# Kernel optimization log

Hardware: AMD Instinct MI355X
Metric: run time of the kernel (lower is better)

The kernel has to match this reference:

```python
import jax, jax.numpy as jnp
from jax import lax
import numpy as np

B, S, IN = 8, 4096, 64
D, H, K = 512, 8, 3
TCN_CH = [256, 256, 512]
HD = D // H


def setup_inputs() -> dict:
    key = jax.random.key(0)
    ks = iter(jax.random.split(key, 64))
    def nrm(shape, s=0.02):
        return jax.random.normal(next(ks), shape, jnp.float32) * s
    inp = {"x": jax.random.normal(next(ks), (B, S, IN), jnp.float32)}
    inp["W_in"] = nrm((IN, D)); inp["b_in"] = jnp.zeros((D,), jnp.float32)
    chans = [D] + TCN_CH
    for i in range(3):
        cin, cout = chans[i], chans[i + 1]
        inp[f"c1w{i}"] = nrm((cout, cin, K), 0.01); inp[f"c1b{i}"] = jnp.zeros((cout,), jnp.float32)
        inp[f"c2w{i}"] = nrm((cout, cout, K), 0.01); inp[f"c2b{i}"] = jnp.zeros((cout,), jnp.float32)
        if cin != cout:  # downsample 1x1 conv (blocks 0 and 2)
            inp[f"dsw{i}"] = nrm((cout, cin, 1), 0.01); inp[f"dsb{i}"] = jnp.zeros((cout,), jnp.float32)
    inp["W_tcn"] = nrm((TCN_CH[-1], D)); inp["b_tcn"] = jnp.zeros((D,), jnp.float32)
    NL = 2  # attention layers, stacked on leading axis
    for n in ["Wq", "Wk", "Wv", "Wo"]:
        inp[n] = nrm((NL, D, D))
    for n in ["bq", "bk", "bv", "bo", "ln_b"]:
        inp[n] = jnp.zeros((NL, D), jnp.float32)
    inp["ln_g"] = jnp.ones((NL, D), jnp.float32)
    inp["W_out"] = nrm((D, 1)); inp["b_out"] = jnp.zeros((1,), jnp.float32)
    return inp


def _conv(x, w, b, dil, pad):
    # x: (B,C,L), w: (O,I,K)
    y = lax.conv_general_dilated(x, w, (1,), [(pad, pad)], rhs_dilation=(dil,),
                                 dimension_numbers=("NCH", "OIH", "NCH"))
    return y + b[None, :, None]


def _block(t, c1w, c1b, c2w, c2b, ds, dil):
    # TemporalConvBlock: symmetric padding (k-1)*dil on both convs, truncate to input length
    pad = (K - 1) * dil
    o = jax.nn.relu(_conv(t, c1w, c1b, dil, pad))   # length L + pad
    o = _conv(o, c2w, c2b, dil, pad)                # length L + 2*pad
    r = t if ds is None else _conv(t, ds[0], ds[1], 1, 0)
    return jax.nn.relu(o[:, :, : t.shape[2]] + r)


def _layernorm(x, g, b, eps=1e-5):
    mu = x.mean(-1, keepdims=True)
    var = ((x - mu) ** 2).mean(-1, keepdims=True)
    return (x - mu) * lax.rsqrt(var + eps) * g + b


def _forward(x, W_in, b_in, c1w0, c1b0, c2w0, c2b0, dsw0, dsb0,
             c1w1, c1b1, c2w1, c2b1, c1w2, c1b2, c2w2, c2b2, dsw2, dsb2,
             W_tcn, b_tcn, Wq, bq, Wk, bk, Wv, bv, Wo, bo, ln_g, ln_b, W_out, b_out):
    h = x @ W_in + b_in                              # (B,S,D)
    t = jnp.swapaxes(h, 1, 2)                        # (B,D,S)
    t = _block(t, c1w0, c1b0, c2w0, c2b0, (dsw0, dsb0), 1)
    t = _block(t, c1w1, c1b1, c2w1, c2b1, None, 2)
    t = _block(t, c1w2, c1b2, c2w2, c2b2, (dsw2, dsb2), 4)
    h = h + jnp.swapaxes(t, 1, 2) @ W_tcn + b_tcn
    # sinusoidal positional encoding
    pos = jnp.arange(S, dtype=jnp.float32)[:, None]
    div = jnp.exp(jnp.arange(0, D, 2, dtype=jnp.float32) * (-np.log(10000.0) / D))
    pe = jnp.stack([jnp.sin(pos * div), jnp.cos(pos * div)], axis=-1).reshape(S, D)
    h = h + pe[None]
    for l in range(Wq.shape[0]):
        res = h
        def heads(y):  # (B,S,D) -> (B,H,S,HD)
            return y.reshape(B, S, H, HD).transpose(0, 2, 1, 3)
        q = heads(h @ Wq[l] + bq[l])
        k = heads(h @ Wk[l] + bk[l])
        v = heads(h @ Wv[l] + bv[l])
        qf = jax.nn.elu(q) + 1.0
        kf = jax.nn.elu(k) + 1.0
        kv = jnp.einsum("bhnd,bhnm->bhdm", kf, v)            # (B,H,HD,HD)
        out = jnp.einsum("bhnd,bhdm->bhnm", qf, kv)          # (B,H,S,HD)
        norm = jnp.maximum(jnp.einsum("bhnd,bhd->bhn", qf, kf.sum(2)), 1e-6)
        out = out / norm[..., None]
        out = out.transpose(0, 2, 1, 3).reshape(B, S, D)
        h = _layernorm(res + out @ Wo[l] + bo[l], ln_g[l], ln_b[l])
    pooled = h.mean(1)                                       # (B,D)
    return (pooled @ W_out + b_out)[:, 0]                    # (B,)


def reference(x, W_in, b_in, c1w0, c1b0, c2w0, c2b0, dsw0, dsb0,
              c1w1, c1b1, c2w1, c2b1, c1w2, c1b2, c2w2, c2b2, dsw2, dsb2,
              W_tcn, b_tcn, Wq, bq, Wk, bk, Wv, bv, Wo, bo, ln_g, ln_b, W_out, b_out):
    return _forward(x, W_in, b_in, c1w0, c1b0, c2w0, c2b0, dsw0, dsb0,
                    c1w1, c1b1, c2w1, c2b1, c1w2, c1b2, c2w2, c2b2, dsw2, dsb2,
                    W_tcn, b_tcn, Wq, bq, Wk, bk, Wv, bv, Wo, bo, ln_g, ln_b, W_out, b_out)
```

## Files before the change

### kernel.cpp

```cpp
#include <hip/hip_runtime.h>

typedef unsigned short u16;
typedef unsigned int u32;
typedef short bhalf8 __attribute__((ext_vector_type(8)));
typedef float f32x4 __attribute__((ext_vector_type(4)));

#define S_LEN 4096
#define NSEG 30

__device__ __forceinline__ float b2f(u16 h){ return __uint_as_float(((u32)h) << 16); }
__device__ __forceinline__ u16 f2b(float f){
  u32 u = __float_as_uint(f);
  return (u16)((u + 0x7FFFu + ((u >> 16) & 1u)) >> 16);
}
__device__ __forceinline__ u32 cvtpk(float a, float b){
  u32 r; asm("v_cvt_pk_bf16_f32 %0, %1, %2" : "=v"(r) : "v"(a), "v"(b)); return r;
}
__device__ __forceinline__ void unp8(uint4 v, float* f){
  f[0]=__uint_as_float(v.x<<16); f[1]=__uint_as_float(v.x&0xffff0000u);
  f[2]=__uint_as_float(v.y<<16); f[3]=__uint_as_float(v.y&0xffff0000u);
  f[4]=__uint_as_float(v.z<<16); f[5]=__uint_as_float(v.z&0xffff0000u);
  f[6]=__uint_as_float(v.w<<16); f[7]=__uint_as_float(v.w&0xffff0000u);
}
__device__ __forceinline__ void unp4(uint2 v, float* f){
  f[0]=__uint_as_float(v.x<<16); f[1]=__uint_as_float(v.x&0xffff0000u);
  f[2]=__uint_as_float(v.y<<16); f[3]=__uint_as_float(v.y&0xffff0000u);
}

__device__ __forceinline__ size_t taddr(int r, int c, int C){
  return (size_t)(r >> 7) * ((size_t)C << 7) + (size_t)((c >> 5) << 12)
       + ((r & 127) << 5) + (c & 31);
}

__device__ __forceinline__ void gload16(const void* g, void* l){
  __builtin_amdgcn_global_load_lds(
      (__attribute__((address_space(1))) void*)(g),
      (__attribute__((address_space(3))) void*)(l), 16, 0, 0);
}

struct PrepArgs {
  const float* src[NSEG];
  int N[NSEG]; int K[NSEG]; int sn[NSEG]; int sk[NSEG]; unsigned off[NSEG];
};

__global__ __launch_bounds__(256) void prep_w(PrepArgs pa, u16* __restrict__ wb){
  int seg = blockIdx.y;
  int N = pa.N[seg], K = pa.K[seg];
  int ntk = (K + 31) >> 5;
  int tiles = ((N + 31) >> 5) * ntk;
  int tile = blockIdx.x;
  if (tile >= tiles) return;
  int n0 = (tile / ntk) << 5, k0 = (tile % ntk) << 5;
  const float* src = pa.src[seg];
  long sn = pa.sn[seg], sk = pa.sk[seg];
  u16* dst = wb + pa.off[seg];
  int lk = threadIdx.x & 31, ln = threadIdx.x >> 5;
  #pragma unroll
  for (int i = 0; i < 4; ++i){
    int n = n0 + ln + i*8, k = k0 + lk;
    if (n < N && k < K)
      dst[(size_t)n*K + k] = f2b(src[(long)n*sn + (long)k*sk]);
  }
}

__global__ __launch_bounds__(256) void pe_k(float* __restrict__ pe){
  int id = blockIdx.x*256 + threadIdx.x;
  int s = id >> 8, i = id & 255;
  float div = expf((float)i * (-2.0f * 9.210340371976184f / 512.0f));
  float a = (float)s * div;
  pe[(size_t)s*512 + 2*i]   = sinf(a);
  pe[(size_t)s*512 + 2*i+1] = cosf(a);
}

__global__ __launch_bounds__(256) void cvt_k(const float* __restrict__ x, u16* __restrict__ xb, int n){
  int id = blockIdx.x*256 + threadIdx.x;
  if (id < n){
    int r = id >> 6, c = id & 63;
    xb[taddr(r, c, 64)] = f2b(x[id]);
  }
}

template<int NTAPS, int KS1, int KS2>
__global__ __launch_bounds__(256) void gemm_k(
    const u16* __restrict__ A, const u16* __restrict__ W,
    const u16* __restrict__ A2, const u16* __restrict__ W2,
    const float* __restrict__ bias, const float* __restrict__ bias2,
    const float* __restrict__ bias3,
    u16* __restrict__ out, const u16* __restrict__ resb,
    const float* __restrict__ peb, const float* __restrict__ den,
    int N, int CA, int CA2, int dil, int nN, int wbstride, int flags)
{
  constexpr bool MT   = (NTAPS == 3);
  constexpr int HALO  = MT ? 8 : 0;
  constexpr int AR    = MT ? 144 : 128;
  constexpr int DA    = (!MT) ? 4 : ((KS2 > 0) ? 4 : 2);
  constexpr int K     = KS1 << 5;
  constexpr int K2    = KS2 << 5;
  constexpr int TOTAL = MT ? (3*KS1 + KS2) : (KS1 + KS2);
  __shared__ u16 As[DA][AR*32];
  __shared__ u16 Bs[4][128*32];
  const int tid = threadIdx.x;
  const int wave = tid >> 6, lane = tid & 63;
  const int wm = wave >> 1, wn = wave & 1;

  const int nwg = gridDim.x;
  const int lin = blockIdx.x;
  const int swz = (lin & 7) * (nwg >> 3) + (lin >> 3);
  const int mb = swz / nN, nb = swz - mb * nN;
  const int m0 = mb << 7, n0 = nb << 7;
  const bool bnd = (m0 & (S_LEN - 1)) == 0;

  const u16* Ae = (flags & 16) ? (A + (((size_t)(n0 & 511) >> 5) << 12)) : A;

  const int lr4 = lane >> 2, lc4 = lane & 3;
  const int c0 = lane >> 4, fro = lane & 15;

  const f32x4 zf = {0.f, 0.f, 0.f, 0.f};
  const bhalf8 zb = {0,0,0,0,0,0,0,0};
  f32x4 acc[4][4];
  #pragma unroll
  for (int i=0;i<4;++i)
    #pragma unroll
    for (int j=0;j<4;++j) acc[i][j] = zf;

  const u16* Wb = W + (size_t)(m0 >> 12) * (size_t)wbstride;
  const size_t abase  = (size_t)mb * ((size_t)CA  << 7);
  const size_t abase2 = (size_t)mb * ((size_t)CA2 << 7);

  auto STAGE_A = [&](int kb, int ab){
    const size_t tb = abase + ((size_t)kb << 12);
    #pragma unroll
    for (int half = 0; half < 2; ++half){
      int mrow = (wave << 5) + (half << 4) + lr4;
      int i = mrow + HALO;
      int cg = lc4 ^ ((i >> 1) & 3);
      gload16(Ae + tb + mrow*32 + (cg << 3), &As[ab][(HALO + (wave << 5) + (half << 4)) * 32]);
    }
    if (MT && wave == 0 && lane < 32){
      int j = lr4;
      int cg = lc4 ^ ((j >> 1) & 3);
      size_t hb_ = (mb ? abase - ((size_t)CA << 7) : abase) + ((size_t)kb << 12) + (120 + j)*32;
      gload16(Ae + hb_ + (cg << 3), &As[ab][0]);
    }
  };
  auto STAGE_A2 = [&](int t2, int ab){
    const size_t tb = abase2 + ((size_t)t2 << 12);
    #pragma unroll
    for (int half = 0; half < 2; ++half){
      int mrow = (wave << 5) + (half << 4) + lr4;
      int i = mrow + HALO;
      int cg = lc4 ^ ((i >> 1) & 3);
      gload16(A2 + tb + mrow*32 + (cg << 3), &As[ab][(HALO + (wave << 5) + (half << 4)) * 32]);
    }
  };
  auto STAGE_B = [&](const u16* Wt, size_t kstride, int kb, int bb){
    #pragma unroll
    for (int half = 0; half < 2; ++half){
      int i = (wave << 5) + (half << 4) + lr4;
      int cg = lc4 ^ ((i >> 1) & 3);
      gload16(Wt + (size_t)(n0 + i) * kstride + (kb << 5) + (cg << 3),
              &Bs[bb][((wave << 5) + (half << 4)) * 32]);
    }
  };
  auto DO16 = [&](int ab, int bb, int sh, bool mask){
    bhalf8 af[4], bf[4];
    #pragma unroll
    for (int mt = 0; mt < 4; ++mt){
      int r8 = (wm << 6) + (mt << 4) + fro + HALO + sh;
      af[mt] = *(const bhalf8*)&As[ab][r8 * 32 + ((c0 ^ ((r8 >> 1) & 3)) << 3)];
    }
    if (MT && mask && bnd && wm == 0 && fro + sh < 0) af[0] = zb;
    #pragma unroll
    for (int nt = 0; nt < 4; ++nt){
      int rB = (wn << 6) + (nt << 4) + fro;
      bf[nt] = *(const bhalf8*)&Bs[bb][rB * 32 + ((c0 ^ ((rB >> 1) & 3)) << 3)];
    }
    #pragma unroll
    for (int mt = 0; mt < 4; ++mt)
      #pragma unroll
      for (int nt = 0; nt < 4; ++nt)
        acc[mt][nt] = __builtin_amdgcn_mfma_f32_16x16x32_bf16(bf[nt], af[mt], acc[mt][nt], 0, 0, 0);
  };

  if constexpr (!MT){
    auto STG = [&](int s){
      int b = s & 3;
      if (s < KS1){ STAGE_A(s, b); STAGE_B(Wb, (size_t)K, s, b); }
      else if (KS2 > 0){ STAGE_A2(s - KS1, b); STAGE_B(W2, (size_t)K2, s - KS1, b); }
    };
    STG(0);
    if constexpr (TOTAL > 1) STG(1);
    if constexpr (TOTAL > 2) STG(2);
    #pragma unroll
    for (int s = 0; s < TOTAL; ++s){
      if (s + 1 >= TOTAL)      asm volatile("s_waitcnt vmcnt(0)" ::: "memory");
      else if (s + 2 >= TOTAL) asm volatile("s_waitcnt vmcnt(4)" ::: "memory");
      else                     asm volatile("s_waitcnt vmcnt(8)" ::: "memory");
      __builtin_amdgcn_sched_barrier(0);
      __builtin_amdgcn_s_barrier();
      __builtin_amdgcn_sched_barrier(0);
      if (s + 3 < TOTAL) STG(s + 3);
      DO16(s & 3, s & 3, 0, false);
    }
  } else {
    auto STG = [&](int s){
      if (s < 3*KS1){
        int kb = s / 3, tap = s % 3;
        if (tap == 0) STAGE_A(kb, kb & (DA-1));
        STAGE_B(Wb + (size_t)tap * N * K, (size_t)K, kb, s & 3);
      } else if (KS2 > 0){
        int t2 = s - 3*KS1;
        STAGE_A2(t2, (KS1 + t2) & (DA-1));
        STAGE_B(W2, (size_t)K2, t2, s & 3);
      }
    };
    STG(0);
    if constexpr (TOTAL > 1) STG(1);
    if constexpr (TOTAL > 2) STG(2);
    #pragma unroll
    for (int s = 0; s < TOTAL; ++s){
      if (s + 1 >= TOTAL)      asm volatile("s_waitcnt vmcnt(0)" ::: "memory");
      else if (s + 2 >= TOTAL) asm volatile("s_waitcnt vmcnt(2)" ::: "memory");
      else                     asm volatile("s_waitcnt vmcnt(4)" ::: "memory");
      __builtin_amdgcn_sched_barrier(0);
      __builtin_amdgcn_s_barrier();
      __builtin_amdgcn_sched_barrier(0);
      if (s + 3 < TOTAL) STG(s + 3);
      if (s < 3*KS1) DO16((s/3) & (DA-1), s & 3, ((s%3) - 2) * dil, true);
      else           DO16((KS1 + (s - 3*KS1)) & (DA-1), s & 3, 0, false);
    }
  }

  const int mb_l = (wm << 6) + fro;
  const int cb_l = (wn << 6) + (c0 << 2);
  const int th = n0 >> 9;
  #pragma unroll
  for (int mt = 0; mt < 4; ++mt){
    const int row = m0 + mb_l + (mt << 4);
    const size_t prow = (size_t)(row & (S_LEN - 1)) * 512;
    #pragma unroll
    for (int nt = 0; nt < 4; ++nt){
      const int col = n0 + cb_l + (nt << 4);
      float v0 = acc[mt][nt][0], v1 = acc[mt][nt][1], v2 = acc[mt][nt][2], v3 = acc[mt][nt][3];
      if (flags & 32){
        const float* bp = (th == 0) ? bias : ((th == 1) ? bias2 : bias3);
        if (bp){ float4 b4 = *(const float4*)&bp[col & 511]; v0+=b4.x; v1+=b4.y; v2+=b4.z; v3+=b4.w; }
      } else {
        if (bias) { float4 b4 = *(const float4*)&bias[col];  v0+=b4.x; v1+=b4.y; v2+=b4.z; v3+=b4.w; }
        if (bias2){ float4 b4 = *(const float4*)&bias2[col]; v0+=b4.x; v1+=b4.y; v2+=b4.z; v3+=b4.w; }
      }
      if (flags & 4){
        uint2 rv = *(const uint2*)(resb + taddr(row, col, N));
        float rf[4]; unp4(rv, rf);
        v0 += rf[0]; v1 += rf[1]; v2 += rf[2]; v3 += rf[3];
      }
      if (flags & 8){
        float4 p4 = *(const float4*)&peb[prow + col];
        v0 += p4.x; v1 += p4.y; v2 += p4.z; v3 += p4.w;
      }
      if (flags & 16){
        float d = fmaxf(den[((size_t)row << 3) + (col >> 6)], 1e-6f);
        float rd = 1.0f / d;
        v0 *= rd; v1 *= rd; v2 *= rd; v3 *= rd;
      }
      if (flags & 1){
        v0 = fmaxf(v0, 0.f); v1 = fmaxf(v1, 0.f); v2 = fmaxf(v2, 0.f); v3 = fmaxf(v3, 0.f);
      }
      if ((flags & 2) && (!(flags & 32) || th < 2)){
        v0 = (v0 > 0.f) ? (v0 + 1.f) : __expf(v0);
        v1 = (v1 > 0.f) ? (v1 + 1.f) : __expf(v1);
        v2 = (v2 > 0.f) ? (v2 + 1.f) : __expf(v2);
        v3 = (v3 > 0.f) ? (v3 + 1.f) : __expf(v3);
      }
      uint2 pk; pk.x = cvtpk(v0, v1); pk.y = cvtpk(v2, v3);
      *(uint2*)(out + taddr(row, col, N)) = pk;
    }
  }
}

__global__ __launch_bounds__(256) void kv_partial(
    const u16* __restrict__ qkv,
    float* __restrict__ kvp, float* __restrict__ ksp)
{
  const int bh = blockIdx.x;
  const int b = bh >> 3, h = bh & 7;
  const int ch = blockIdx.y;
  const int t = threadIdx.x;
  __shared__ u16 kfs[16][64];
  __shared__ u16 vs[16][64];
  float acc[4][4] = {{0.f}};
  float ks[4] = {0.f,0.f,0.f,0.f};
  const int d0 = (t >> 4) << 2;
  const int c0 = (t & 15) << 2;
  const int lr = t >> 4, lc = (t & 15) << 2;
  const int rowbase = (b << 12) + (ch << 9);
  const int ck = 512 + (h << 6) + lc;
  const int cv = 1024 + (h << 6) + lc;
  for (int g = 0; g < 32; ++g){
    int r = rowbase + (g << 4) + lr;
    *(uint2*)&kfs[lr][lc] = *(const uint2*)(qkv + taddr(r, ck, 1536));
    *(uint2*)&vs[lr][lc]  = *(const uint2*)(qkv + taddr(r, cv, 1536));
    __syncthreads();
    #pragma unroll
    for (int i = 0; i < 16; ++i){
      float kv4[4], vv4[4];
      unp4(*(const uint2*)&kfs[i][d0], kv4);
      unp4(*(const uint2*)&vs[i][c0], vv4);
      #pragma unroll
      for (int j=0;j<4;++j)
        #pragma unroll
        for (int k2=0;k2<4;++k2) acc[j][k2] += kv4[j]*vv4[k2];
      if ((t & 15) == 0){
        #pragma unroll
        for (int j=0;j<4;++j) ks[j] += kv4[j];
      }
    }
    __syncthreads();
  }
  float* dst = kvp + ((size_t)(bh << 3) + ch) * 4096;
  #pragma unroll
  for (int j=0;j<4;++j)
    #pragma unroll
    for (int k2=0;k2<4;++k2) dst[(d0+j)*64 + (c0+k2)] = acc[j][k2];
  if ((t & 15) == 0){
    float* kd = ksp + ((size_t)(bh << 3) + ch) * 64;
    #pragma unroll
    for (int j=0;j<4;++j) kd[d0+j] = ks[j];
  }
}

__global__ __launch_bounds__(256) void kvred_k(
    const float* __restrict__ kvp, const float* __restrict__ ksp,
    float* __restrict__ kvf, float* __restrict__ ksf)
{
  int bh = blockIdx.x, t = threadIdx.x;
  for (int e = t; e < 4096; e += 256){
    float s = 0.f;
    #pragma unroll
    for (int ch = 0; ch < 8; ++ch) s += kvp[((size_t)(bh<<3)+ch)*4096 + e];
    kvf[(size_t)bh*4096 + e] = s;
  }
  if (t < 64){
    float s = 0.f;
    #pragma unroll
    for (int ch = 0; ch < 8; ++ch) s += ksp[((size_t)(bh<<3)+ch)*64 + t];
    ksf[bh*64 + t] = s;
  }
}

__global__ __launch_bounds__(256) void den_k(const u16* __restrict__ qkv,
    const float* __restrict__ ksf, float* __restrict__ den)
{
  int id = blockIdx.x*256 + threadIdx.x;
  int r = id >> 3, h = id & 7;
  int b = r >> 12;
  const float* ks = ksf + ((b<<3)+h)*64;
  float s = 0.f;
  for (int d = 0; d < 64; d += 8){
    uint4 vq = *(const uint4*)(qkv + taddr(r, (h << 6) + d, 1536));
    float f[8]; unp8(vq, f);
    #pragma unroll
    for (int j=0;j<8;++j) s += f[j]*ks[d+j];
  }
  den[id] = s;
}

__global__ __launch_bounds__(256) void packkv2_k(const float* __restrict__ kvf, u16* __restrict__ wbd){
  int id = blockIdx.x*256 + threadIdx.x;
  int b = id >> 16;
  int n = (id >> 7) & 511, j = id & 127;
  float v = 0.f;
  if ((j >> 6) == ((n >> 6) & 1))
    v = kvf[((size_t)((b<<3)+(n>>6)))*4096 + (j & 63)*64 + (n & 63)];
  wbd[id] = f2b(v);
}

__global__ __launch_bounds__(256) void ln_k(const u16* __restrict__ in,
    const float* __restrict__ g, const float* __restrict__ beta, u16* __restrict__ out)
{
  int wave = threadIdx.x >> 6, lane = threadIdx.x & 63;
  int row = blockIdx.x*4 + wave;
  size_t ad = taddr(row, lane*8, 512);
  uint4 pv = *(const uint4*)(in + ad);
  float f[8]; unp8(pv, f);
  float s = 0.f, ss = 0.f;
  #pragma unroll
  for (int i=0;i<8;++i){ s += f[i]; ss += f[i]*f[i]; }
  for (int m=1;m<64;m<<=1){ s += __shfl_xor(s,m); ss += __shfl_xor(ss,m); }
  float mean = s * (1.f/512.f);
  float var = ss * (1.f/512.f) - mean*mean;
  float rstd = rsqrtf(fmaxf(var, 0.f) + 1e-5f);
  u16 o[8];
  #pragma unroll
  for (int i=0;i<8;++i){
    int c = lane*8 + i;
    o[i] = f2b((f[i]-mean)*rstd*g[c] + beta[c]);
  }
  *(uint4*)(out + ad) = *(uint4*)o;
}

__global__ __launch_bounds__(256) void pool1_k(const u16* __restrict__ hb,
    const float* __restrict__ wout, float* __restrict__ part)
{
  int b = blockIdx.x >> 6, ch = blockIdx.x & 63;
  int t = threadIdx.x;
  __shared__ float ws[512];
  for (int i=t;i<512;i+=256) ws[i] = wout[i];
  __syncthreads();
  int r = (b << 12) + (ch << 6) + (t >> 2);
  int c0 = (t & 3) << 7;
  float s = 0.f;
  for (int i=0;i<128;i+=8){
    uint4 v = *(const uint4*)(hb + taddr(r, c0 + i, 512));
    float f[8]; unp8(v, f);
    #pragma unroll
    for (int j=0;j<8;++j) s += f[j]*ws[c0+i+j];
  }
  __shared__ float red[256];
  red[t] = s; __syncthreads();
  for (int k=128;k;k>>=1){ if (t<k) red[t]+=red[t+k]; __syncthreads(); }
  if (!t) part[blockIdx.x] = red[0];
}

__global__ __launch_bounds__(64) void pool2_k(const float* __restrict__ part,
    const float* __restrict__ bout, float* __restrict__ out)
{
  int b = blockIdx.x, t = threadIdx.x;
  float s = part[(b << 6) + t];
  for (int m=1;m<64;m<<=1) s += __shfl_xor(s,m);
  if (!t) out[b] = s * (1.f/4096.f) + bout[0];
}

extern "C" void kernel_launch(void* const* d_in, const int* in_sizes, int n_in,
                              void* d_out, int out_size, void* d_ws, size_t ws_size,
                              hipStream_t stream)
{
  (void)in_sizes; (void)n_in; (void)out_size; (void)ws_size;
  const float* x    = (const float*)d_in[0];
  const float* W_in = (const float*)d_in[1];
  const float* b_in = (const float*)d_in[2];
  const float* c1w0 = (const float*)d_in[3];
  const float* c1b0 = (const float*)d_in[4];
  const float* c2w0 = (const float*)d_in[5];
  const float* c2b0 = (const float*)d_in[6];
  const float* dsw0 = (const float*)d_in[7];
  const float* dsb0 = (const float*)d_in[8];
  const float* c1w1 = (const float*)d_in[9];
  const float* c1b1 = (const float*)d_in[10];
  const float* c2w1 = (const float*)d_in[11];
  const float* c2b1 = (const float*)d_in[12];
  const float* c1w2 = (const float*)d_in[13];
  const float* c1b2 = (const float*)d_in[14];
  const float* c2w2 = (const float*)d_in[15];
  const float* c2b2 = (const float*)d_in[16];
  const float* dsw2 = (const float*)d_in[17];
  const float* dsb2 = (const float*)d_in[18];
  const float* W_tcn= (const float*)d_in[19];
  const float* b_tcn= (const float*)d_in[20];
  const float* Wq   = (const float*)d_in[21];
  const float* Wk   = (const float*)d_in[22];
  const float* Wv   = (const float*)d_in[23];
  const float* Wo   = (const float*)d_in[24];
  const float* bq   = (const float*)d_in[25];
  const float* bk   = (const float*)d_in[26];
  const float* bv   = (const float*)d_in[27];
  const float* bo   = (const float*)d_in[28];
  const float* lnb  = (const float*)d_in[29];
  const float* lng  = (const float*)d_in[30];
  const float* W_out= (const float*)d_in[31];
  const float* b_out= (const float*)d_in[32];

  char* base = (char*)d_ws;
  size_t off = 0;
  auto alloc = [&](size_t bytes) -> void* {
    void* p = base + off;
    off += (bytes + 255) & ~(size_t)255;
    return p;
  };
  u16* WB   = (u16*)alloc(4816896ull*2);
  u16* wbd  = (u16*)alloc(8ull*512*128*2);
  float* peb= (float*)alloc(4096ull*512*4);
  float* den= (float*)alloc(32768ull*8*4);
  float* kvp= (float*)alloc(512ull*4096*4);
  float* ksp= (float*)alloc(512ull*64*4);
  float* kvf= (float*)alloc(64ull*4096*4);
  float* ksf= (float*)alloc(64ull*64*4);
  float* part=(float*)alloc(512*4);
  u16* hb   = (u16*)alloc(32768ull*512*2);
  char* qkvR= (char*)alloc(32768ull*1536*2);
  u16* atto = (u16*)alloc(32768ull*512*2);

  u16* qkvb = (u16*)qkvR;
  u16* xb   = (u16*)(qkvR);
  u16* t1b  = (u16*)(qkvR + 4194304);
  u16* t2b  = (u16*)(qkvR + 20971520);
  u16* t3b  = (u16*)(qkvR + 37748736);
  u16* o1b  = atto;

  unsigned wo_ = 0;
  auto wseg = [&](unsigned e){ unsigned o = wo_; wo_ += e; return o; };
  unsigned oWin  = wseg(512*64);
  unsigned oC1w0 = wseg(3*256*512);
  unsigned oC2w0 = wseg(3*256*256);
  unsigned oDs0  = wseg(256*512);
  unsigned oC1w1 = wseg(3*256*256);
  unsigned oC2w1 = wseg(3*256*256);
  unsigned oC1w2 = wseg(3*512*256);
  unsigned oC2w2 = wseg(3*512*512);
  unsigned oDs2  = wseg(512*256);
  unsigned oWtcn = wseg(512*512);
  unsigned oQKV  = wseg(2*1536*512);
  unsigned oWo   = wseg(2*512*512);

  PrepArgs pa;
  int si = 0;
  auto seg = [&](const float* s, int N, int K, int sn, int sk, unsigned o){
    pa.src[si]=s; pa.N[si]=N; pa.K[si]=K; pa.sn[si]=sn; pa.sk[si]=sk; pa.off[si]=o; ++si;
  };
  seg(W_in, 512, 64, 1, 512, oWin);
  for (int t=0;t<3;++t) seg(c1w0 + t, 256, 512, 1536, 3, oC1w0 + t*131072);
  for (int t=0;t<3;++t) seg(c2w0 + t, 256, 256,  768, 3, oC2w0 + t*65536);
  seg(dsw0, 256, 512, 512, 1, oDs0);
  for (int t=0;t<3;++t) seg(c1w1 + t, 256, 256,  768, 3, oC1w1 + t*65536);
  for (int t=0;t<3;++t) seg(c2w1 + t, 256, 256,  768, 3, oC2w1 + t*65536);
  for (int t=0;t<3;++t) seg(c1w2 + t, 512, 256,  768, 3, oC1w2 + t*131072);
  for (int t=0;t<3;++t) seg(c2w2 + t, 512, 512, 1536, 3, oC2w2 + t*262144);
  seg(dsw2, 512, 256, 256, 1, oDs2);
  seg(W_tcn, 512, 512, 1, 512, oWtcn);
  for (int l=0;l<2;++l){
    seg(Wq + l*262144, 512, 512, 1, 512, oQKV + l*786432 + 0);
    seg(Wk + l*262144, 512, 512, 1, 512, oQKV + l*786432 + 262144);
    seg(Wv + l*262144, 512, 512, 1, 512, oQKV + l*786432 + 524288);
  }
  for (int l=0;l<2;++l) seg(Wo + l*262144, 512, 512, 1, 512, oWo + l*262144);

  prep_w<<<dim3(256, NSEG), 256, 0, stream>>>(pa, WB);
  pe_k<<<4096, 256, 0, stream>>>(peb);
  cvt_k<<<8192, 256, 0, stream>>>(x, xb, 32768*64);

  const int RELU=1, ELU1=2, RES=4, PE=8, DIV=16, QKV=32;
  auto gemm = [&](const u16* A, const u16* W, const u16* A2, const u16* W2,
                  const float* b1, const float* b2, const float* b3,
                  u16* out, const u16* resb,
                  int K, int K2, int N, int CA, int CA2, int ntaps,
                  int dil, int wbs, int flags){
    int nN = N >> 7;
    dim3 grid(256 * nN);
    if (ntaps == 3){
      if (K == 512 && K2 == 0)
        gemm_k<3,16,0><<<grid, 256, 0, stream>>>(A, W, A2, W2, b1, b2, b3, out, resb,
                                                 peb, den, N, CA, CA2, dil, nN, wbs, flags);
      else if (K == 256 && K2 == 512)
        gemm_k<3,8,16><<<grid, 256, 0, stream>>>(A, W, A2, W2, b1, b2, b3, out, resb,
                                                 peb, den, N, CA, CA2, dil, nN, wbs, flags);
      else if (K == 256 && K2 == 0)
        gemm_k<3,8,0><<<grid, 256, 0, stream>>>(A, W, A2, W2, b1, b2, b3, out, resb,
                                                peb, den, N, CA, CA2, dil, nN, wbs, flags);
      else
        gemm_k<3,16,8><<<grid, 256, 0, stream>>>(A, W, A2, W2, b1, b2, b3, out, resb,
                                                 peb, den, N, CA, CA2, dil, nN, wbs, flags);
    } else {
      if (K == 64)
        gemm_k<1,2,0><<<grid, 256, 0, stream>>>(A, W, A2, W2, b1, b2, b3, out, resb,
                                                peb, den, N, CA, CA2, dil, nN, wbs, flags);
      else if (K == 128)
        gemm_k<1,4,0><<<grid, 256, 0, stream>>>(A, W, A2, W2, b1, b2, b3, out, resb,
                                                peb, den, N, CA, CA2, dil, nN, wbs, flags);
      else
        gemm_k<1,16,0><<<grid, 256, 0, stream>>>(A, W, A2, W2, b1, b2, b3, out, resb,
                                                 peb, den, N, CA, CA2, dil, nN, wbs, flags);
    }
  };

  gemm(xb, WB + oWin, nullptr, nullptr, b_in, nullptr, nullptr, hb, nullptr,
       64, 0, 512, 64, 0, 1, 1, 0, 0);
  gemm(hb,  WB + oC1w0, nullptr, nullptr, c1b0, nullptr, nullptr, o1b, nullptr,
       512, 0, 256, 512, 0, 3, 1, 0, RELU);
  gemm(o1b, WB + oC2w0, hb, WB + oDs0, c2b0, dsb0, nullptr, t1b, nullptr,
       256, 512, 256, 256, 512, 3, 1, 0, RELU);
  gemm(t1b, WB + oC1w1, nullptr, nullptr, c1b1, nullptr, nullptr, o1b, nullptr,
       256, 0, 256, 256, 0, 3, 2, 0, RELU);
  gemm(o1b, WB + oC2w1, nullptr, nullptr, c2b1, nullptr, nullptr, t2b, t1b,
       256, 0, 256, 256, 0, 3, 2, 0, RELU|RES);
  gemm(t2b, WB + oC1w2, nullptr, nullptr, c1b2, nullptr, nullptr, o1b, nullptr,
       256, 0, 512, 256, 0, 3, 4, 0, RELU);
  gemm(o1b, WB + oC2w2, t2b, WB + oDs2, c2b2, dsb2, nullptr, t3b, nullptr,
       512, 256, 512, 512, 256, 3, 4, 0, RELU);
  gemm(t3b, WB + oWtcn, nullptr, nullptr, b_tcn, nullptr, nullptr, hb, hb,
       512, 0, 512, 512, 0, 1, 1, 0, RES|PE);

  for (int l = 0; l < 2; ++l){
    gemm(hb, WB + oQKV + l*786432, nullptr, nullptr, bq + l*512, bk + l*512, bv + l*512,
         qkvb, nullptr, 512, 0, 1536, 512, 0, 1, 1, 0, ELU1|QKV);
    kv_partial<<<dim3(64, 8), 256, 0, stream>>>(qkvb, kvp, ksp);
    kvred_k<<<64, 256, 0, stream>>>(kvp, ksp, kvf, ksf);
    den_k<<<1024, 256, 0, stream>>>(qkvb, ksf, den);
    packkv2_k<<<2048, 256, 0, stream>>>(kvf, wbd);
    gemm(qkvb, wbd, nullptr, nullptr, nullptr, nullptr, nullptr, atto, nullptr,
         128, 0, 512, 1536, 0, 1, 1, 512*128, DIV);
    gemm(atto, WB + oWo + l*262144, nullptr, nullptr, bo + l*512, nullptr, nullptr, hb, hb,
         512, 0, 512, 512, 0, 1, 1, 0, RES);
    ln_k<<<8192, 256, 0, stream>>>(hb, lng + l*512, lnb + l*512, hb);
  }

  pool1_k<<<512, 256, 0, stream>>>(hb, W_out, part);
  pool2_k<<<8, 64, 0, stream>>>(part, b_out, (float*)d_out);
}
```

Measured before the change: 832.2 us.

## Fuse final LayerNorm into pooling and shrink non-tap GEMM pipeline to 3 stages

The last layer's LayerNorm is folded into the pooling kernel. Each row's mean and variance are computed there, and gamma and beta are folded algebraically into the output weights, so one full read-modify-write pass over the activations is skipped. Separately, the single-tap GEMM pipeline drops from 4 to 3 shared-memory buffers (prefetch depth 2) to reduce LDS use and possibly raise occupancy, at the cost of less latency hiding. The pooled result now uses an unrounded fp32 normalization instead of bf16-rounded LN outputs.

Result: faster. 781.9 us (-6.0%).

```diff
diff --git a/kernel.cpp b/kernel.cpp
--- a/kernel.cpp
+++ b/kernel.cpp
@@ -93,12 +93,13 @@
   constexpr bool MT   = (NTAPS == 3);
   constexpr int HALO  = MT ? 8 : 0;
   constexpr int AR    = MT ? 144 : 128;
-  constexpr int DA    = (!MT) ? 4 : ((KS2 > 0) ? 4 : 2);
+  constexpr int DA    = (!MT) ? 3 : ((KS2 > 0) ? 4 : 2);
+  constexpr int DB    = MT ? 4 : 3;
   constexpr int K     = KS1 << 5;
   constexpr int K2    = KS2 << 5;
   constexpr int TOTAL = MT ? (3*KS1 + KS2) : (KS1 + KS2);
   __shared__ u16 As[DA][AR*32];
-  __shared__ u16 Bs[4][128*32];
+  __shared__ u16 Bs[DB][128*32];
   const int tid = threadIdx.x;
   const int wave = tid >> 6, lane = tid & 63;
   const int wm = wave >> 1, wn = wave & 1;
@@ -184,23 +185,21 @@
 
   if constexpr (!MT){
     auto STG = [&](int s){
-      int b = s & 3;
+      int b = s % 3;
       if (s < KS1){ STAGE_A(s, b); STAGE_B(Wb, (size_t)K, s, b); }
       else if (KS2 > 0){ STAGE_A2(s - KS1, b); STAGE_B(W2, (size_t)K2, s - KS1, b); }
     };
     STG(0);
     if constexpr (TOTAL > 1) STG(1);
-    if constexpr (TOTAL > 2) STG(2);
     #pragma unroll
     for (int s = 0; s < TOTAL; ++s){
-      if (s + 1 >= TOTAL)      asm volatile("s_waitcnt vmcnt(0)" ::: "memory");
-      else if (s + 2 >= TOTAL) asm volatile("s_waitcnt vmcnt(4)" ::: "memory");
-      else                     asm volatile("s_waitcnt vmcnt(8)" ::: "memory");
+      if (s + 1 >= TOTAL) asm volatile("s_waitcnt vmcnt(0)" ::: "memory");
+      else                asm volatile("s_waitcnt vmcnt(4)" ::: "memory");
       __builtin_amdgcn_sched_barrier(0);
       __builtin_amdgcn_s_barrier();
       __builtin_amdgcn_sched_barrier(0);
-      if (s + 3 < TOTAL) STG(s + 3);
-      DO16(s & 3, s & 3, 0, false);
+      if (s + 2 < TOTAL) STG(s + 2);
+      DO16(s % 3, s % 3, 0, false);
     }
   } else {
     auto STG = [&](int s){
@@ -400,25 +399,50 @@
 }
 
 __global__ __launch_bounds__(256) void pool1_k(const u16* __restrict__ hb,
-    const float* __restrict__ wout, float* __restrict__ part)
+    const float* __restrict__ wout, const float* __restrict__ g,
+    const float* __restrict__ beta, float* __restrict__ part)
 {
   int b = blockIdx.x >> 6, ch = blockIdx.x & 63;
   int t = threadIdx.x;
   __shared__ float ws[512];
-  for (int i=t;i<512;i+=256) ws[i] = wout[i];
+  __shared__ float red[256];
+  __shared__ float S2[2];
+  float a0 = 0.f, a1 = 0.f;
+  for (int i = t; i < 512; i += 256){
+    float w = wout[i];
+    float gw = w * g[i];
+    ws[i] = gw;
+    a0 += gw;
+    a1 += w * beta[i];
+  }
+  red[t] = a0; __syncthreads();
+  for (int k2=128;k2;k2>>=1){ if (t<k2) red[t]+=red[t+k2]; __syncthreads(); }
+  if (!t) S2[0] = red[0];
   __syncthreads();
+  red[t] = a1; __syncthreads();
+  for (int k2=128;k2;k2>>=1){ if (t<k2) red[t]+=red[t+k2]; __syncthreads(); }
+  if (!t) S2[1] = red[0];
+  __syncthreads();
+  const float Sgw = S2[0], Sbw = S2[1];
+
   int r = (b << 12) + (ch << 6) + (t >> 2);
   int c0 = (t & 3) << 7;
-  float s = 0.f;
-  for (int i=0;i<128;i+=8){
+  float sd = 0.f, s1 = 0.f, s2 = 0.f;
+  for (int i = 0; i < 128; i += 8){
     uint4 v = *(const uint4*)(hb + taddr(r, c0 + i, 512));
     float f[8]; unp8(v, f);
     #pragma unroll
-    for (int j=0;j<8;++j) s += f[j]*ws[c0+i+j];
-  }
-  __shared__ float red[256];
-  red[t] = s; __syncthreads();
-  for (int k=128;k;k>>=1){ if (t<k) red[t]+=red[t+k]; __syncthreads(); }
+    for (int j=0;j<8;++j){ float x = f[j]; sd += x*ws[c0+i+j]; s1 += x; s2 += x*x; }
+  }
+  sd += __shfl_xor(sd,1); s1 += __shfl_xor(s1,1); s2 += __shfl_xor(s2,1);
+  sd += __shfl_xor(sd,2); s1 += __shfl_xor(s1,2); s2 += __shfl_xor(s2,2);
+  float mean = s1 * (1.f/512.f);
+  float var  = s2 * (1.f/512.f) - mean*mean;
+  float rstd = rsqrtf(fmaxf(var, 0.f) + 1e-5f);
+  float rowv = rstd * (sd - mean * Sgw) + Sbw;
+  red[t] = ((t & 3) == 0) ? rowv : 0.f;
+  __syncthreads();
+  for (int k2=128;k2;k2>>=1){ if (t<k2) red[t]+=red[t+k2]; __syncthreads(); }
   if (!t) part[blockIdx.x] = red[0];
 }
 
@@ -600,9 +624,10 @@
          128, 0, 512, 1536, 0, 1, 1, 512*128, DIV);
     gemm(atto, WB + oWo + l*262144, nullptr, nullptr, bo + l*512, nullptr, nullptr, hb, hb,
          512, 0, 512, 512, 0, 1, 1, 0, RES);
-    ln_k<<<8192, 256, 0, stream>>>(hb, lng + l*512, lnb + l*512, hb);
-  }
-
-  pool1_k<<<512, 256, 0, stream>>>(hb, W_out, part);
+    if (l == 0)
+      ln_k<<<8192, 256, 0, stream>>>(hb, lng, lnb, hb);
+  }
+
+  pool1_k<<<512, 256, 0, stream>>>(hb, W_out, lng + 512, lnb + 512, part);
   pool2_k<<<8, 64, 0, stream>>>(part, b_out, (float*)d_out);
 }
```
